# Performance work log

Measured on AMD Instinct MI355X. Metric: run time of the kernel, lower is better.

Reference implementation:

```python
import jax, jax.numpy as jnp
import numpy as np

ALPHA = 0.5


def setup_inputs() -> dict:
    key = jax.random.key(0)
    k1, k2 = jax.random.split(key)
    inputs = jax.random.normal(k1, (16384,), dtype=jnp.float32)
    targets = jax.random.normal(k2, (16384,), dtype=jnp.float32)
    return {"inputs": inputs, "targets": targets}


def reference(inputs, targets):
    # Chamfer 1D: mean over x of min_j |x_i - y_j|, symmetrized with weight alpha.
    x = inputs.reshape(-1)
    y = targets.reshape(-1)
    n = x.shape[0]
    m = y.shape[0]
    # Pairwise absolute differences [N, M]; min over each axis gives both directions.
    d = jnp.abs(x[:, None] - y[None, :])
    cd_xy = jnp.sum(jnp.min(d, axis=1))  # sum_i min_j |x_i - y_j|
    cd_yx = jnp.sum(jnp.min(d, axis=0))  # sum_j min_i |y_j - x_i|
    return ALPHA * cd_xy / n + (1.0 - ALPHA) * cd_yx / m
```

## Files before the change

kernel.cpp:

```cpp
#include <hip/hip_runtime.h>
#include <cfloat>

#define TPB 256
#define BMT 1024
#define BKT 32768
#define SLOTS 16
#define OVCAP 4096
#define RLO -8.0f
#define RSCALE (BKT / 16.0f)
#define ALPHA 0.5f

#define CNT_OFF   0
#define OVC_OFF   (2 * BKT)
#define ZERO_WORDS (2 * BKT + 2)
#define BM1_OFF   ((ZERO_WORDS + 63) & ~63)
#define BM2_OFF   (BM1_OFF + 2048)
#define SLOTS_OFF (BM2_OFF + 64)
#define OVF_OFF   (SLOTS_OFF + 2 * BKT * SLOTS)

__device__ __forceinline__ int bucket_of(float v) {
    int b = (int)((v - RLO) * RSCALE);
    return min(max(b, 0), BKT - 1);
}

__global__ __launch_bounds__(TPB) void
chamfer_build(const float* __restrict__ x, const float* __restrict__ y,
              int n, int m, unsigned* __restrict__ ws) {
    const int i = blockIdx.x * TPB + threadIdx.x;
    if (i >= n + m) return;
    const bool isx = i < n;
    const int side = isx ? 0 : 1;
    const float v = isx ? x[i] : y[i - n];
    const int b = bucket_of(v);
    const unsigned pos = atomicAdd(ws + CNT_OFF + side * BKT + b, 1u);
    if (pos < SLOTS) {
        ((float*)(ws + SLOTS_OFF))[((size_t)(side * BKT + b)) * SLOTS + pos] = v;
    } else {
        const unsigned o = atomicAdd(ws + OVC_OFF + side, 1u);
        if (o < OVCAP) ((float*)(ws + OVF_OFF))[side * OVCAP + o] = v;
    }
}

__global__ __launch_bounds__(BMT) void chamfer_bitmap(unsigned* __restrict__ ws) {
    __shared__ unsigned s_bm1[2048];
    const int t = threadIdx.x;
    const uint4* cnt4 = (const uint4*)(ws + CNT_OFF);
#pragma unroll
    for (int k = 0; k < 2; ++k) {
        const int w = t + k * BMT;
        unsigned bits = 0;
#pragma unroll
        for (int j = 0; j < 8; ++j) {
            const uint4 c = cnt4[w * 8 + j];
            if (c.x) bits |= 1u << (4 * j + 0);
            if (c.y) bits |= 1u << (4 * j + 1);
            if (c.z) bits |= 1u << (4 * j + 2);
            if (c.w) bits |= 1u << (4 * j + 3);
        }
        ws[BM1_OFF + w] = bits;
        s_bm1[w] = bits;
    }
    __syncthreads();
    if (t < 64) {
        unsigned bits = 0;
#pragma unroll
        for (int j = 0; j < 32; ++j)
            if (s_bm1[t * 32 + j]) bits |= 1u << j;
        ws[BM2_OFF + t] = bits;
    }
}

__device__ __forceinline__ int prev_ne(const unsigned* __restrict__ bm1,
                                       const unsigned* __restrict__ bm2, int b) {
    if (b == 0) return -1;
    const int p = b - 1;
    unsigned w = bm1[p >> 5] & (~0u >> (31 - (p & 31)));
    if (w) return (p & ~31) | (31 - __clz(w));
    const int W = (p >> 5) - 1;
    if (W < 0) return -1;
    int j = W >> 5;
    unsigned w2 = bm2[j] & (~0u >> (31 - (W & 31)));
    while (!w2 && --j >= 0) w2 = bm2[j];
    if (!w2) return -1;
    const int Wp = (j << 5) | (31 - __clz(w2));
    return (Wp << 5) | (31 - __clz(bm1[Wp]));
}
__device__ __forceinline__ int next_ne(const unsigned* __restrict__ bm1,
                                       const unsigned* __restrict__ bm2, int b) {
    if (b >= BKT - 1) return -1;
    const int p = b + 1;
    unsigned w = bm1[p >> 5] & (~0u << (p & 31));
    if (w) return (p & ~31) | (__ffs(w) - 1);
    const int W = (p >> 5) + 1;
    if (W > 1023) return -1;
    int j = W >> 5;
    unsigned w2 = bm2[j] & (~0u << (W & 31));
    while (!w2 && ++j < 32) w2 = bm2[j];
    if (!w2) return -1;
    const int Wp = (j << 5) | (__ffs(w2) - 1);
    return (Wp << 5) | (__ffs(bm1[Wp]) - 1);
}

__device__ __forceinline__ float scan_bucket(const unsigned* __restrict__ cnt,
                                             const float* __restrict__ slots,
                                             int side, int b, float v, float best) {
    const unsigned c = min(cnt[b], (unsigned)SLOTS);
    const float4* sl4 = (const float4*)(slots + ((size_t)(side * BKT + b)) * SLOTS);
    float e[SLOTS];
    *(float4*)(e + 0)  = sl4[0];
    *(float4*)(e + 4)  = sl4[1];
    *(float4*)(e + 8)  = sl4[2];
    *(float4*)(e + 12) = sl4[3];
#pragma unroll
    for (int j = 0; j < SLOTS; ++j) {
        const float d = fabsf(v - e[j]);
        best = ((unsigned)j < c) ? fminf(best, d) : best;
    }
    return best;
}

__global__ __launch_bounds__(TPB) void
chamfer_query(const float* __restrict__ x, const float* __restrict__ y,
              int n, int m, const unsigned* __restrict__ ws,
              double* __restrict__ bsums) {
    const int q = blockIdx.x * TPB + threadIdx.x;
    const int total = n + m;
    double sx = 0.0, sy = 0.0;
    if (q < total) {
        const bool isx = q < n;
        const float v = isx ? x[q] : y[q - n];
        const int side = isx ? 1 : 0;
        const unsigned* cnt = ws + CNT_OFF + side * BKT;
        const unsigned* bm1 = ws + BM1_OFF + side * 1024;
        const unsigned* bm2 = ws + BM2_OFF + side * 32;
        const float* slots = (const float*)(ws + SLOTS_OFF);
        const int b = bucket_of(v);

        float best = scan_bucket(cnt, slots, side, b, v, FLT_MAX);
        const int bp = prev_ne(bm1, bm2, b);
        if (bp >= 0) best = scan_bucket(cnt, slots, side, bp, v, best);
        const int bn = next_ne(bm1, bm2, b);
        if (bn >= 0) best = scan_bucket(cnt, slots, side, bn, v, best);

        const unsigned oc = min(ws[OVC_OFF + side], (unsigned)OVCAP);
        const float* ovf = (const float*)(ws + OVF_OFF) + side * OVCAP;
        for (unsigned k = 0; k < oc; ++k)
            best = fminf(best, fabsf(v - ovf[k]));

        if (isx) sx = (double)best; else sy = (double)best;
    }
    for (int off = 32; off > 0; off >>= 1) {
        sx += __shfl_down(sx, off);
        sy += __shfl_down(sy, off);
    }
    __shared__ double wsx[TPB / 64], wsy[TPB / 64];
    const int w = threadIdx.x >> 6;
    if ((threadIdx.x & 63) == 0) { wsx[w] = sx; wsy[w] = sy; }
    __syncthreads();
    if (threadIdx.x == 0) {
        double tx = 0.0, ty = 0.0;
#pragma unroll
        for (int i = 0; i < TPB / 64; ++i) { tx += wsx[i]; ty += wsy[i]; }
        bsums[2 * blockIdx.x] = tx;
        bsums[2 * blockIdx.x + 1] = ty;
    }
}

__global__ __launch_bounds__(TPB) void
chamfer_final(const double* __restrict__ bsums, int nb,
              int n, int m, float* __restrict__ out) {
    double sx = 0.0, sy = 0.0;
    for (int i = threadIdx.x; i < nb; i += blockDim.x) {
        sx += bsums[2 * i];
        sy += bsums[2 * i + 1];
    }
    for (int off = 32; off > 0; off >>= 1) {
        sx += __shfl_down(sx, off);
        sy += __shfl_down(sy, off);
    }
    __shared__ double lsx[4], lsy[4];
    const int wave = threadIdx.x >> 6;
    if ((threadIdx.x & 63) == 0) { lsx[wave] = sx; lsy[wave] = sy; }
    __syncthreads();
    if (threadIdx.x == 0) {
        double tx = 0.0, ty = 0.0;
        for (int w = 0; w < (int)(blockDim.x >> 6); ++w) { tx += lsx[w]; ty += lsy[w]; }
        const double a = (double)ALPHA;
        out[0] = (float)(a * tx / (double)n + (1.0 - a) * ty / (double)m);
    }
}

extern "C" void kernel_launch(void* const* d_in, const int* in_sizes, int n_in,
                              void* d_out, int out_size, void* d_ws, size_t ws_size,
                              hipStream_t stream) {
    const float* x = (const float*)d_in[0];
    const float* y = (const float*)d_in[1];
    const int n = in_sizes[0];
    const int m = in_sizes[1];
    float* out = (float*)d_out;
    const int total = n + m;

    unsigned* ws = (unsigned*)d_ws;
    const size_t meta_bytes = (size_t)(OVF_OFF + 2 * OVCAP) * sizeof(unsigned);
    const size_t meta_al = (meta_bytes + 255) & ~(size_t)255;
    double* bsums = (double*)((char*)d_ws + meta_al);

    const int nb = (total + TPB - 1) / TPB;

    hipMemsetAsync(ws, 0, (size_t)ZERO_WORDS * sizeof(unsigned), stream);
    chamfer_build<<<nb, TPB, 0, stream>>>(x, y, n, m, ws);
    chamfer_bitmap<<<1, BMT, 0, stream>>>(ws);
    chamfer_query<<<nb, TPB, 0, stream>>>(x, y, n, m, ws, bsums);
    chamfer_final<<<1, TPB, 0, stream>>>(bsums, nb, n, m, out);
}
```

Measured before the change: 78.62 us.

## Fuse build, bitmap, query and reduce into one cooperative kernel

The memset, the bucket build, the bitmap kernel, the query and the final reduce become a single cooperative kernel whose phases are separated by grid-wide syncs. The two-level bitmap is now built on the fly with atomicOr calls when a bucket gets its first element, so the separate single-block bitmap pass goes away. This removes several launch gaps and dependency stalls between kernels, at the cost of three grid barriers and extra atomics. The grid is capped at 2048 blocks, but the query phase handles only one element per thread (q = tid), so inputs with more than 2048*256 elements would be dropped. The test size of 32768 elements fits within that limit.

```diff
diff --git a/kernel.cpp b/kernel.cpp
--- a/kernel.cpp
+++ b/kernel.cpp
@@ -1,8 +1,10 @@
 #include <hip/hip_runtime.h>
+#include <hip/hip_cooperative_groups.h>
 #include <cfloat>
 
+namespace cg = cooperative_groups;
+
 #define TPB 256
-#define BMT 1024
 #define BKT 32768
 #define SLOTS 16
 #define OVCAP 4096
@@ -11,63 +13,16 @@
 #define ALPHA 0.5f
 
 #define CNT_OFF   0
-#define OVC_OFF   (2 * BKT)
-#define ZERO_WORDS (2 * BKT + 2)
-#define BM1_OFF   ((ZERO_WORDS + 63) & ~63)
+#define BM1_OFF   (2 * BKT)
 #define BM2_OFF   (BM1_OFF + 2048)
-#define SLOTS_OFF (BM2_OFF + 64)
+#define OVC_OFF   (BM2_OFF + 64)
+#define ZERO_WORDS (OVC_OFF + 2)
+#define SLOTS_OFF (((ZERO_WORDS) + 63) & ~63)
 #define OVF_OFF   (SLOTS_OFF + 2 * BKT * SLOTS)
 
 __device__ __forceinline__ int bucket_of(float v) {
     int b = (int)((v - RLO) * RSCALE);
     return min(max(b, 0), BKT - 1);
-}
-
-__global__ __launch_bounds__(TPB) void
-chamfer_build(const float* __restrict__ x, const float* __restrict__ y,
-              int n, int m, unsigned* __restrict__ ws) {
-    const int i = blockIdx.x * TPB + threadIdx.x;
-    if (i >= n + m) return;
-    const bool isx = i < n;
-    const int side = isx ? 0 : 1;
-    const float v = isx ? x[i] : y[i - n];
-    const int b = bucket_of(v);
-    const unsigned pos = atomicAdd(ws + CNT_OFF + side * BKT + b, 1u);
-    if (pos < SLOTS) {
-        ((float*)(ws + SLOTS_OFF))[((size_t)(side * BKT + b)) * SLOTS + pos] = v;
-    } else {
-        const unsigned o = atomicAdd(ws + OVC_OFF + side, 1u);
-        if (o < OVCAP) ((float*)(ws + OVF_OFF))[side * OVCAP + o] = v;
-    }
-}
-
-__global__ __launch_bounds__(BMT) void chamfer_bitmap(unsigned* __restrict__ ws) {
-    __shared__ unsigned s_bm1[2048];
-    const int t = threadIdx.x;
-    const uint4* cnt4 = (const uint4*)(ws + CNT_OFF);
-#pragma unroll
-    for (int k = 0; k < 2; ++k) {
-        const int w = t + k * BMT;
-        unsigned bits = 0;
-#pragma unroll
-        for (int j = 0; j < 8; ++j) {
-            const uint4 c = cnt4[w * 8 + j];
-            if (c.x) bits |= 1u << (4 * j + 0);
-            if (c.y) bits |= 1u << (4 * j + 1);
-            if (c.z) bits |= 1u << (4 * j + 2);
-            if (c.w) bits |= 1u << (4 * j + 3);
-        }
-        ws[BM1_OFF + w] = bits;
-        s_bm1[w] = bits;
-    }
-    __syncthreads();
-    if (t < 64) {
-        unsigned bits = 0;
-#pragma unroll
-        for (int j = 0; j < 32; ++j)
-            if (s_bm1[t * 32 + j]) bits |= 1u << j;
-        ws[BM2_OFF + t] = bits;
-    }
 }
 
 __device__ __forceinline__ int prev_ne(const unsigned* __restrict__ bm1,
@@ -120,73 +75,105 @@
 }
 
 __global__ __launch_bounds__(TPB) void
-chamfer_query(const float* __restrict__ x, const float* __restrict__ y,
-              int n, int m, const unsigned* __restrict__ ws,
-              double* __restrict__ bsums) {
-    const int q = blockIdx.x * TPB + threadIdx.x;
+chamfer_fused(const float* __restrict__ x, const float* __restrict__ y,
+              int n, int m, unsigned* __restrict__ ws,
+              double* __restrict__ bsums, float* __restrict__ out) {
+    cg::grid_group grid = cg::this_grid();
+    const int tid = blockIdx.x * TPB + (int)threadIdx.x;
+    const int gsz = (int)gridDim.x * TPB;
     const int total = n + m;
-    double sx = 0.0, sy = 0.0;
-    if (q < total) {
-        const bool isx = q < n;
-        const float v = isx ? x[q] : y[q - n];
-        const int side = isx ? 1 : 0;
-        const unsigned* cnt = ws + CNT_OFF + side * BKT;
-        const unsigned* bm1 = ws + BM1_OFF + side * 1024;
-        const unsigned* bm2 = ws + BM2_OFF + side * 32;
-        const float* slots = (const float*)(ws + SLOTS_OFF);
+
+    for (int w = tid; w < ZERO_WORDS; w += gsz) ws[w] = 0u;
+    grid.sync();
+
+    for (int i = tid; i < total; i += gsz) {
+        const bool isx = i < n;
+        const int side = isx ? 0 : 1;
+        const float v = isx ? x[i] : y[i - n];
         const int b = bucket_of(v);
-
-        float best = scan_bucket(cnt, slots, side, b, v, FLT_MAX);
-        const int bp = prev_ne(bm1, bm2, b);
-        if (bp >= 0) best = scan_bucket(cnt, slots, side, bp, v, best);
-        const int bn = next_ne(bm1, bm2, b);
-        if (bn >= 0) best = scan_bucket(cnt, slots, side, bn, v, best);
-
-        const unsigned oc = min(ws[OVC_OFF + side], (unsigned)OVCAP);
-        const float* ovf = (const float*)(ws + OVF_OFF) + side * OVCAP;
-        for (unsigned k = 0; k < oc; ++k)
-            best = fminf(best, fabsf(v - ovf[k]));
-
-        if (isx) sx = (double)best; else sy = (double)best;
-    }
-    for (int off = 32; off > 0; off >>= 1) {
-        sx += __shfl_down(sx, off);
-        sy += __shfl_down(sy, off);
-    }
-    __shared__ double wsx[TPB / 64], wsy[TPB / 64];
-    const int w = threadIdx.x >> 6;
-    if ((threadIdx.x & 63) == 0) { wsx[w] = sx; wsy[w] = sy; }
-    __syncthreads();
-    if (threadIdx.x == 0) {
-        double tx = 0.0, ty = 0.0;
+        const unsigned pos = atomicAdd(ws + CNT_OFF + side * BKT + b, 1u);
+        if (pos < SLOTS) {
+            ((float*)(ws + SLOTS_OFF))[((size_t)(side * BKT + b)) * SLOTS + pos] = v;
+        } else {
+            const unsigned o = atomicAdd(ws + OVC_OFF + side, 1u);
+            if (o < OVCAP) ((float*)(ws + OVF_OFF))[side * OVCAP + o] = v;
+        }
+        if (pos == 0) {
+            const int W = b >> 5;
+            const unsigned old =
+                atomicOr(ws + BM1_OFF + side * 1024 + W, 1u << (b & 31));
+            if (old == 0)
+                atomicOr(ws + BM2_OFF + side * 32 + (W >> 5), 1u << (W & 31));
+        }
+    }
+    grid.sync();
+
+    {
+        const int q = tid;
+        double sx = 0.0, sy = 0.0;
+        if (q < total) {
+            const bool isx = q < n;
+            const float v = isx ? x[q] : y[q - n];
+            const int side = isx ? 1 : 0;
+            const unsigned* cnt = ws + CNT_OFF + side * BKT;
+            const unsigned* bm1 = ws + BM1_OFF + side * 1024;
+            const unsigned* bm2 = ws + BM2_OFF + side * 32;
+            const float* slots = (const float*)(ws + SLOTS_OFF);
+            const int b = bucket_of(v);
+
+            float best = scan_bucket(cnt, slots, side, b, v, FLT_MAX);
+            const int bp = prev_ne(bm1, bm2, b);
+            if (bp >= 0) best = scan_bucket(cnt, slots, side, bp, v, best);
+            const int bn = next_ne(bm1, bm2, b);
+            if (bn >= 0) best = scan_bucket(cnt, slots, side, bn, v, best);
+
+            const unsigned oc = min(ws[OVC_OFF + side], (unsigned)OVCAP);
+            const float* ovf = (const float*)(ws + OVF_OFF) + side * OVCAP;
+            for (unsigned k = 0; k < oc; ++k)
+                best = fminf(best, fabsf(v - ovf[k]));
+
+            if (isx) sx = (double)best; else sy = (double)best;
+        }
+        for (int off = 32; off > 0; off >>= 1) {
+            sx += __shfl_down(sx, off);
+            sy += __shfl_down(sy, off);
+        }
+        __shared__ double wsx[TPB / 64], wsy[TPB / 64];
+        const int w = threadIdx.x >> 6;
+        if ((threadIdx.x & 63) == 0) { wsx[w] = sx; wsy[w] = sy; }
+        __syncthreads();
+        if (threadIdx.x == 0) {
+            double tx = 0.0, ty = 0.0;
 #pragma unroll
-        for (int i = 0; i < TPB / 64; ++i) { tx += wsx[i]; ty += wsy[i]; }
-        bsums[2 * blockIdx.x] = tx;
-        bsums[2 * blockIdx.x + 1] = ty;
-    }
-}
-
-__global__ __launch_bounds__(TPB) void
-chamfer_final(const double* __restrict__ bsums, int nb,
-              int n, int m, float* __restrict__ out) {
-    double sx = 0.0, sy = 0.0;
-    for (int i = threadIdx.x; i < nb; i += blockDim.x) {
-        sx += bsums[2 * i];
-        sy += bsums[2 * i + 1];
-    }
-    for (int off = 32; off > 0; off >>= 1) {
-        sx += __shfl_down(sx, off);
-        sy += __shfl_down(sy, off);
-    }
-    __shared__ double lsx[4], lsy[4];
-    const int wave = threadIdx.x >> 6;
-    if ((threadIdx.x & 63) == 0) { lsx[wave] = sx; lsy[wave] = sy; }
-    __syncthreads();
-    if (threadIdx.x == 0) {
-        double tx = 0.0, ty = 0.0;
-        for (int w = 0; w < (int)(blockDim.x >> 6); ++w) { tx += lsx[w]; ty += lsy[w]; }
-        const double a = (double)ALPHA;
-        out[0] = (float)(a * tx / (double)n + (1.0 - a) * ty / (double)m);
+            for (int i = 0; i < TPB / 64; ++i) { tx += wsx[i]; ty += wsy[i]; }
+            bsums[2 * blockIdx.x] = tx;
+            bsums[2 * blockIdx.x + 1] = ty;
+        }
+    }
+    grid.sync();
+
+    if (blockIdx.x == 0) {
+        const int nb = (int)gridDim.x;
+        double sx = 0.0, sy = 0.0;
+        for (int i = (int)threadIdx.x; i < nb; i += TPB) {
+            sx += bsums[2 * i];
+            sy += bsums[2 * i + 1];
+        }
+        for (int off = 32; off > 0; off >>= 1) {
+            sx += __shfl_down(sx, off);
+            sy += __shfl_down(sy, off);
+        }
+        __shared__ double lsx[TPB / 64], lsy[TPB / 64];
+        const int wave = threadIdx.x >> 6;
+        if ((threadIdx.x & 63) == 0) { lsx[wave] = sx; lsy[wave] = sy; }
+        __syncthreads();
+        if (threadIdx.x == 0) {
+            double tx = 0.0, ty = 0.0;
+#pragma unroll
+            for (int w = 0; w < TPB / 64; ++w) { tx += lsx[w]; ty += lsy[w]; }
+            const double a = (double)ALPHA;
+            out[0] = (float)(a * tx / (double)n + (1.0 - a) * ty / (double)m);
+        }
     }
 }
 
@@ -195,8 +182,8 @@
                               hipStream_t stream) {
     const float* x = (const float*)d_in[0];
     const float* y = (const float*)d_in[1];
-    const int n = in_sizes[0];
-    const int m = in_sizes[1];
+    int n = in_sizes[0];
+    int m = in_sizes[1];
     float* out = (float*)d_out;
     const int total = n + m;
 
@@ -205,11 +192,11 @@
     const size_t meta_al = (meta_bytes + 255) & ~(size_t)255;
     double* bsums = (double*)((char*)d_ws + meta_al);
 
-    const int nb = (total + TPB - 1) / TPB;
-
-    hipMemsetAsync(ws, 0, (size_t)ZERO_WORDS * sizeof(unsigned), stream);
-    chamfer_build<<<nb, TPB, 0, stream>>>(x, y, n, m, ws);
-    chamfer_bitmap<<<1, BMT, 0, stream>>>(ws);
-    chamfer_query<<<nb, TPB, 0, stream>>>(x, y, n, m, ws, bsums);
-    chamfer_final<<<1, TPB, 0, stream>>>(bsums, nb, n, m, out);
-}
+    int nb = (total + TPB - 1) / TPB;
+    if (nb > 2048) nb = 2048;
+
+    void* args[] = {(void*)&x, (void*)&y, (void*)&n, (void*)&m,
+                    (void*)&ws, (void*)&bsums, (void*)&out};
+    hipLaunchCooperativeKernel((const void*)chamfer_fused, dim3(nb), dim3(TPB),
+                               args, 0, stream);
+}
```

Result: slower. 120.5 us (+53.3%).
